# Performance work log

Hardware: AMD Instinct MI355X
Metric: run time of the kernel (lower is better)

Reference implementation:

```python
import jax, jax.numpy as jnp
import numpy as np

SCALE = 65536          # Q16.16 fixed point, matching the torch module's SCALE
N_SEGMENTS = 16


def setup_inputs() -> dict:
    key = jax.random.key(0)
    k1, k2, k3, k4, k5 = jax.random.split(key, 5)
    # Large activation tensor -> memory-bound elementwise bucketize+affine.
    x = jax.random.normal(k1, (32, 4096, 1024), dtype=jnp.float32) * 2.0
    # n_segments-1 interior breakpoints, sorted, Q16.16 covering ~[-4, 4].
    breakpoints = jnp.sort(
        jax.random.randint(k2, (N_SEGMENTS - 1,), -4 * SCALE, 4 * SCALE, dtype=jnp.int32)
    )
    # Per-segment intercepts in Q16.16, within +/- 1.0 real units.
    intercepts = jax.random.randint(k3, (N_SEGMENTS,), -SCALE, SCALE, dtype=jnp.int32)
    # Per-segment slope signs in {-1, +1}.
    signs = 2 * jax.random.randint(k4, (N_SEGMENTS,), 0, 2, dtype=jnp.int32) - 1
    # Per-segment slope exponents: slope magnitude = 2^-exp (arithmetic right shift).
    exps = jax.random.randint(k5, (N_SEGMENTS,), 0, 8, dtype=jnp.int32)
    return {
        "x": x,
        "breakpoints": breakpoints,
        "intercepts": intercepts,
        "signs": signs,
        "exps": exps,
    }


def _plac_int32(x_q16, breakpoints, intercepts, signs, exps):
    # Bucketize each Q16.16 element against the sorted interior breakpoints;
    # seg in [0, n_segments-1].
    seg = jnp.searchsorted(breakpoints, x_q16, side="right").astype(jnp.int32)
    b = jnp.take(intercepts, seg)   # segment intercept (Q16.16)
    s = jnp.take(signs, seg)        # segment sign (+/-1)
    e = jnp.take(exps, seg)         # segment slope exponent
    # y = intercept + sign * (x >> exp) in int32 Q16.16 (arithmetic shift).
    return b + s * jnp.right_shift(x_q16, e)


def reference(x, breakpoints, intercepts, signs, exps):
    # Faithful to torch forward: detach, quantize to Q16.16 int32, eval, dequantize.
    x_q16 = (jax.lax.stop_gradient(x).astype(jnp.float32) * SCALE).astype(jnp.int32)
    y_q16 = _plac_int32(x_q16, breakpoints, intercepts, signs, exps)
    return (y_q16.astype(jnp.float32) / SCALE).astype(x.dtype)
```

## Files before the change

kernel.cpp:

```cpp
#include <hip/hip_runtime.h>

#define NSEG 16

__global__ __launch_bounds__(256) void plac_kernel(
    const float* __restrict__ x,
    const int* __restrict__ bps,
    const int* __restrict__ intercepts,
    const int* __restrict__ signs,
    const int* __restrict__ exps,
    float* __restrict__ out,
    long long n4,
    long long n)
{
    __shared__ int s_bp[15];
    __shared__ int s_b[NSEG];
    __shared__ int s_s[NSEG];
    __shared__ int s_e[NSEG];

    const int tid = threadIdx.x;
    if (tid < 15) s_bp[tid] = bps[tid];
    if (tid < NSEG) {
        s_b[tid] = intercepts[tid];
        s_s[tid] = signs[tid];
        s_e[tid] = exps[tid];
    }
    __syncthreads();

    long long idx    = (long long)blockIdx.x * blockDim.x + tid;
    long long stride = (long long)gridDim.x * blockDim.x;

    const float4* __restrict__ x4 = (const float4*)x;
    float4* __restrict__ o4 = (float4*)out;

    for (long long i = idx; i < n4; i += stride) {
        float4 v = x4[i];
        float4 r;
        float* vp = reinterpret_cast<float*>(&v);
        float* rp = reinterpret_cast<float*>(&r);
        #pragma unroll
        for (int j = 0; j < 4; ++j) {
            int xq = (int)(vp[j] * 65536.0f);
            int seg = 0;
            #pragma unroll
            for (int k = 0; k < 15; ++k) seg += (xq >= s_bp[k]);
            int y = s_b[seg] + s_s[seg] * (xq >> s_e[seg]);
            rp[j] = (float)y * (1.0f / 65536.0f);
        }
        o4[i] = r;
    }

    if (blockIdx.x == 0) {
        long long base = n4 * 4;
        for (long long i = base + tid; i < n; i += blockDim.x) {
            int xq = (int)(x[i] * 65536.0f);
            int seg = 0;
            #pragma unroll
            for (int k = 0; k < 15; ++k) seg += (xq >= s_bp[k]);
            int y = s_b[seg] + s_s[seg] * (xq >> s_e[seg]);
            out[i] = (float)y * (1.0f / 65536.0f);
        }
    }
}

extern "C" void kernel_launch(void* const* d_in, const int* in_sizes, int n_in,
                              void* d_out, int out_size, void* d_ws, size_t ws_size,
                              hipStream_t stream) {
    const float* x          = (const float*)d_in[0];
    const int*   bps        = (const int*)d_in[1];
    const int*   intercepts = (const int*)d_in[2];
    const int*   signs      = (const int*)d_in[3];
    const int*   exps       = (const int*)d_in[4];
    float* out = (float*)d_out;

    long long n  = (long long)out_size;
    long long n4 = n / 4;

    const int block = 256;
    long long blocks_needed = (n4 + block - 1) / block;
    int grid = (int)((blocks_needed < 2048) ? (blocks_needed > 0 ? blocks_needed : 1)
                                            : 2048);

    plac_kernel<<<grid, block, 0, stream>>>(x, bps, intercepts, signs, exps,
                                            out, n4, n);
}
```

Measured before the change: 213.3 us.

## Evaluate PLAC in float math with packed LDS table and nontemporal 2x loads

Replaces the integer quantize/compare/shift path with float arithmetic. Breakpoints are held as floats in registers, and the per-segment intercept, sign and power-of-two scale are packed into one 16-byte LDS entry so a single LDS read serves each element. The main loop is unrolled to process two float4s per iteration, and loads and stores use nontemporal hints to cut instruction overhead and cache pollution. Risks: the float path may differ from the int32 result at large magnitudes or at int overflow edges, and the int-to-float conversion of breakpoints happens per thread.

```diff
diff --git a/kernel.cpp b/kernel.cpp
--- a/kernel.cpp
+++ b/kernel.cpp
@@ -1,6 +1,8 @@
 #include <hip/hip_runtime.h>
 
 #define NSEG 16
+
+typedef float f32x4 __attribute__((ext_vector_type(4)));
 
 __global__ __launch_bounds__(256) void plac_kernel(
     const float* __restrict__ x,
@@ -12,52 +14,82 @@
     long long n4,
     long long n)
 {
-    __shared__ int s_bp[15];
-    __shared__ int s_b[NSEG];
-    __shared__ int s_s[NSEG];
-    __shared__ int s_e[NSEG];
+    __shared__ f32x4 s_tab[NSEG];
 
     const int tid = threadIdx.x;
-    if (tid < 15) s_bp[tid] = bps[tid];
     if (tid < NSEG) {
-        s_b[tid] = intercepts[tid];
-        s_s[tid] = signs[tid];
-        s_e[tid] = exps[tid];
+        float b  = (float)intercepts[tid] * (1.0f / 65536.0f);
+        float s  = (float)signs[tid]      * (1.0f / 65536.0f);
+        float ei = __int_as_float((127 - exps[tid]) << 23);
+        f32x4 row = {b, s, ei, 0.0f};
+        s_tab[tid] = row;
     }
     __syncthreads();
+
+    float bpf[15];
+    #pragma unroll
+    for (int k = 0; k < 15; ++k) bpf[k] = (float)bps[k];
 
     long long idx    = (long long)blockIdx.x * blockDim.x + tid;
     long long stride = (long long)gridDim.x * blockDim.x;
 
-    const float4* __restrict__ x4 = (const float4*)x;
-    float4* __restrict__ o4 = (float4*)out;
+    const f32x4* __restrict__ x4 = (const f32x4*)x;
+    f32x4* __restrict__ o4 = (f32x4*)out;
 
-    for (long long i = idx; i < n4; i += stride) {
-        float4 v = x4[i];
-        float4 r;
-        float* vp = reinterpret_cast<float*>(&v);
-        float* rp = reinterpret_cast<float*>(&r);
+    long long i = idx;
+    for (; i + stride < n4; i += 2 * stride) {
+        f32x4 va = __builtin_nontemporal_load(&x4[i]);
+        f32x4 vb = __builtin_nontemporal_load(&x4[i + stride]);
+        f32x4 ra, rb;
         #pragma unroll
         for (int j = 0; j < 4; ++j) {
-            int xq = (int)(vp[j] * 65536.0f);
+            float t = truncf(va[j] * 65536.0f);
             int seg = 0;
             #pragma unroll
-            for (int k = 0; k < 15; ++k) seg += (xq >= s_bp[k]);
-            int y = s_b[seg] + s_s[seg] * (xq >> s_e[seg]);
-            rp[j] = (float)y * (1.0f / 65536.0f);
+            for (int k = 0; k < 15; ++k) seg += (t >= bpf[k]);
+            f32x4 c = s_tab[seg];
+            float u = floorf(t * c.z);
+            ra[j] = fmaf(c.y, u, c.x);
         }
-        o4[i] = r;
+        #pragma unroll
+        for (int j = 0; j < 4; ++j) {
+            float t = truncf(vb[j] * 65536.0f);
+            int seg = 0;
+            #pragma unroll
+            for (int k = 0; k < 15; ++k) seg += (t >= bpf[k]);
+            f32x4 c = s_tab[seg];
+            float u = floorf(t * c.z);
+            rb[j] = fmaf(c.y, u, c.x);
+        }
+        __builtin_nontemporal_store(ra, &o4[i]);
+        __builtin_nontemporal_store(rb, &o4[i + stride]);
+    }
+    for (; i < n4; i += stride) {
+        f32x4 v = __builtin_nontemporal_load(&x4[i]);
+        f32x4 r;
+        #pragma unroll
+        for (int j = 0; j < 4; ++j) {
+            float t = truncf(v[j] * 65536.0f);
+            int seg = 0;
+            #pragma unroll
+            for (int k = 0; k < 15; ++k) seg += (t >= bpf[k]);
+            f32x4 c = s_tab[seg];
+            float u = floorf(t * c.z);
+            r[j] = fmaf(c.y, u, c.x);
+        }
+        __builtin_nontemporal_store(r, &o4[i]);
     }
 
     if (blockIdx.x == 0) {
         long long base = n4 * 4;
-        for (long long i = base + tid; i < n; i += blockDim.x) {
-            int xq = (int)(x[i] * 65536.0f);
+        for (long long ii = base + tid; ii < n; ii += blockDim.x) {
+            float t = truncf(x[ii] * 65536.0f);
             int seg = 0;
             #pragma unroll
-            for (int k = 0; k < 15; ++k) seg += (xq >= s_bp[k]);
-            int y = s_b[seg] + s_s[seg] * (xq >> s_e[seg]);
-            out[i] = (float)y * (1.0f / 65536.0f);
+            for (int k = 0; k < 15; ++k) seg += (t >= bpf[k]);
+            f32x4 c = s_tab[seg];
+            float u = floorf(t * c.z);
+            out[ii] = fmaf(c.y, u, c.x);
         }
     }
 }
```

Result: slower. 251.2 us (+17.7%).
